# Performance work log

Hardware: AMD Instinct MI355X
Metric: run time of the kernel (lower is better)

## Reference

```python
import jax, jax.numpy as jnp
import numpy as np

B, S, H = 4, 4096, 2880
E, K = 32, 4


def setup_inputs() -> dict:
    key = jax.random.key(0)
    k1, k2 = jax.random.split(key)
    hidden_states = jax.random.normal(k1, (B, S, H), dtype=jnp.float32)
    # router weight, scaled like a typical init (std ~ 1/sqrt(H))
    weight = jax.random.normal(k2, (E, H), dtype=jnp.float32) / np.sqrt(H)
    bias = jnp.zeros((E,), dtype=jnp.float32)
    return {"hidden_states": hidden_states, "weight": weight, "bias": bias}


def reference(hidden_states, weight, bias):
    b, s, h = hidden_states.shape
    x = hidden_states.reshape(-1, h)                     # [T, H]
    logits = jnp.einsum('th,eh->te', x, weight) + bias   # [T, E]
    # select top-k logits (sorted descending), then softmax over the subset
    topk_logits, topk_idx = jax.lax.top_k(logits, K)     # [T, K]
    topk_weight = jax.nn.softmax(topk_logits.astype(jnp.float32), axis=-1)
    return topk_idx, topk_weight
```

## Files before the change

### kernel.cpp

```cpp
#include <hip/hip_runtime.h>
#include <math.h>

#define H_DIM 2880
#define E_NUM 32
#define TOPK 4
#define TT 32
#define KW 96
#define NSTG 30
#define NBUF 3
#define GRP 776
#define XB 0
#define XBS 3104
#define WB 9312
#define WBS 3104
#define SMSZ 18624
#define REDR 36
#define LGTO 4608

#define GLD16(gp, lp)                                                  \
    __builtin_amdgcn_global_load_lds(                                  \
        (const __attribute__((address_space(1))) void*)(gp),           \
        (__attribute__((address_space(3))) void*)(lp), 16, 0, 0)

__global__ __launch_bounds__(256, 2) void gate_fused(
    const float* __restrict__ x, const float* __restrict__ w,
    const float* __restrict__ bias, float* __restrict__ out, int T) {
    __shared__ float sm[SMSZ];
    const int tid = threadIdx.x;
    const int lane = tid & 63;
    const int wq = __builtin_amdgcn_readfirstlane(tid >> 6);
    const int tt = lane & 3;
    const int et = (lane >> 2) & 3;
    const int ksl = lane >> 4;
    const int t0 = blockIdx.x * TT;

    const float* gx[3]; const float* gw[3]; int lx[3], lw[3];
#pragma unroll
    for (int i = 0; i < 3; ++i) {
        const int d = i * 256 + lane * 4;
        const int r = d / KW, kk = d % KW;
        gx[i] = x + (size_t)(t0 + wq * 8 + r) * H_DIM + kk;
        gw[i] = w + (size_t)(wq * 8 + r) * H_DIM + kk;
        lx[i] = XB + wq * GRP + d;
        lw[i] = WB + wq * GRP + d;
    }

    float acc[64];
#pragma unroll
    for (int i = 0; i < 64; ++i) acc[i] = 0.f;

#pragma unroll
    for (int i = 0; i < 3; ++i) GLD16(gx[i], &sm[lx[i]]);
#pragma unroll
    for (int i = 0; i < 3; ++i) GLD16(gw[i], &sm[lw[i]]);
#pragma unroll
    for (int i = 0; i < 3; ++i) GLD16(gx[i] + KW, &sm[lx[i] + XBS]);
#pragma unroll
    for (int i = 0; i < 3; ++i) GLD16(gw[i] + KW, &sm[lw[i] + WBS]);

    const int ks = wq * 4 + ksl;
    const int koA = ks * 4;
    const int koB = 64 + ks * 2;

    int p = 0, pf = 2;
    for (int s = 0; s < NSTG; ++s) {
        if (s + 1 < NSTG) {
            asm volatile("s_waitcnt vmcnt(6)" ::: "memory");
        } else {
            asm volatile("s_waitcnt vmcnt(0)" ::: "memory");
        }
        __builtin_amdgcn_s_barrier();
        asm volatile("" ::: "memory");

        if (s + 2 < NSTG) {
            const size_t go = (size_t)(s + 2) * KW;
            const int xo = pf * XBS, wo = pf * WBS;
#pragma unroll
            for (int i = 0; i < 3; ++i) GLD16(gx[i] + go, &sm[lx[i] + xo]);
#pragma unroll
            for (int i = 0; i < 3; ++i) GLD16(gw[i] + go, &sm[lw[i] + wo]);
        }

        const float* xbp = &sm[XB + p * XBS + tt * GRP];
        const float* wbp = &sm[WB + p * WBS + et * GRP];

        float4 xa[8], wa[8];
#pragma unroll
        for (int i = 0; i < 8; ++i) xa[i] = *(const float4*)(xbp + i * KW + koA);
#pragma unroll
        for (int j = 0; j < 8; ++j) wa[j] = *(const float4*)(wbp + j * KW + koA);
#pragma unroll
        for (int i = 0; i < 8; ++i)
#pragma unroll
            for (int j = 0; j < 8; ++j)
                acc[i * 8 + j] += xa[i].x * wa[j].x + xa[i].y * wa[j].y +
                                  xa[i].z * wa[j].z + xa[i].w * wa[j].w;

        float2 x2[8], w2[8];
#pragma unroll
        for (int i = 0; i < 8; ++i) x2[i] = *(const float2*)(xbp + i * KW + koB);
#pragma unroll
        for (int j = 0; j < 8; ++j) w2[j] = *(const float2*)(wbp + j * KW + koB);
#pragma unroll
        for (int i = 0; i < 8; ++i)
#pragma unroll
            for (int j = 0; j < 8; ++j)
                acc[i * 8 + j] += x2[i].x * w2[j].x + x2[i].y * w2[j].y;

        p = (p == NBUF - 1) ? 0 : p + 1;
        pf = (pf == NBUF - 1) ? 0 : pf + 1;
    }

    __syncthreads();

#pragma unroll
    for (int d = 0; d < 64; ++d) {
        acc[d] += __shfl_xor(acc[d], 16, 64);
        acc[d] += __shfl_xor(acc[d], 32, 64);
    }

    if (ksl == 0) {
#pragma unroll
        for (int i = 0; i < 8; ++i) {
            float* rp = &sm[wq * (TT * REDR) + (tt * 8 + i) * REDR + et * 8];
            *(float4*)(rp + 0) = make_float4(acc[i * 8 + 0], acc[i * 8 + 1],
                                             acc[i * 8 + 2], acc[i * 8 + 3]);
            *(float4*)(rp + 4) = make_float4(acc[i * 8 + 4], acc[i * 8 + 5],
                                             acc[i * 8 + 6], acc[i * 8 + 7]);
        }
    }
    __syncthreads();

    {
        const int tok = tid >> 3, e4 = (tid & 7) * 4;
        float4 sg = *(const float4*)(bias + e4);
#pragma unroll
        for (int q = 0; q < 4; ++q) {
            float4 v = *(const float4*)&sm[q * (TT * REDR) + tok * REDR + e4];
            sg.x += v.x; sg.y += v.y; sg.z += v.z; sg.w += v.w;
        }
        *(float4*)&sm[LGTO + tok * REDR + e4] = sg;
    }
    __syncthreads();

    if (tid < TT) {
        const int t = t0 + tid;
        float logit[E_NUM];
#pragma unroll
        for (int j = 0; j < 8; ++j) {
            float4 v = *(const float4*)&sm[LGTO + tid * REDR + j * 4];
            logit[j * 4] = v.x; logit[j * 4 + 1] = v.y;
            logit[j * 4 + 2] = v.z; logit[j * 4 + 3] = v.w;
        }

        int idx[TOPK];
        float val[TOPK];
#pragma unroll
        for (int k = 0; k < TOPK; ++k) {
            float best = -INFINITY;
            int bi = 0;
#pragma unroll
            for (int e = 0; e < E_NUM; ++e) {
                bool taken = false;
                for (int p2 = 0; p2 < k; ++p2) taken = taken || (idx[p2] == e);
                float v = logit[e];
                if (!taken && v > best) { best = v; bi = e; }
            }
            idx[k] = bi;
            val[k] = best;
        }
        float ex[TOPK], ssum = 0.f;
#pragma unroll
        for (int k = 0; k < TOPK; ++k) { ex[k] = expf(val[k] - val[0]); ssum += ex[k]; }
        const float inv = 1.f / ssum;

        *(float4*)(out + (size_t)t * 4) =
            make_float4((float)idx[0], (float)idx[1], (float)idx[2], (float)idx[3]);
        *(float4*)(out + (size_t)T * 4 + (size_t)t * 4) =
            make_float4(ex[0] * inv, ex[1] * inv, ex[2] * inv, ex[3] * inv);
    }
}

extern "C" void kernel_launch(void* const* d_in, const int* in_sizes, int n_in,
                              void* d_out, int out_size, void* d_ws, size_t ws_size,
                              hipStream_t stream) {
    const float* x    = (const float*)d_in[0];
    const float* w    = (const float*)d_in[1];
    const float* bias = (const float*)d_in[2];
    float* out = (float*)d_out;

    const int T = in_sizes[0] / H_DIM;

    gate_fused<<<dim3(T / TT), 256, 0, stream>>>(x, w, bias, out, T);
}
```

Before: 274.9 us.

## Halve token tile to 16 and double-buffer to raise occupancy

Shrinks the per-block token tile from 32 to 16, which halves accumulators per thread (64 to 32) and roughly halves LDS use. Pipelining drops from a triple buffer with prefetch depth 2 to a double buffer that waits on all loads each stage. Launch bounds go from 2 to 4 blocks per CU, and only two waves load x. The aim is more resident waves to hide memory latency, at the cost of re-reading the router weight twice as often and a shallower prefetch.

```diff
diff --git a/kernel.cpp b/kernel.cpp
--- a/kernel.cpp
+++ b/kernel.cpp
@@ -4,25 +4,23 @@
 #define H_DIM 2880
 #define E_NUM 32
 #define TOPK 4
-#define TT 32
+#define TT 16
 #define KW 96
 #define NSTG 30
-#define NBUF 3
 #define GRP 776
-#define XB 0
-#define XBS 3104
-#define WB 9312
+#define XBS 1552
+#define WB0 3104
 #define WBS 3104
-#define SMSZ 18624
+#define SMSZ 9312
 #define REDR 36
-#define LGTO 4608
+#define LGTO 2304
 
 #define GLD16(gp, lp)                                                  \
     __builtin_amdgcn_global_load_lds(                                  \
         (const __attribute__((address_space(1))) void*)(gp),           \
         (__attribute__((address_space(3))) void*)(lp), 16, 0, 0)
 
-__global__ __launch_bounds__(256, 2) void gate_fused(
+__global__ __launch_bounds__(256, 4) void gate_fused(
     const float* __restrict__ x, const float* __restrict__ w,
     const float* __restrict__ bias, float* __restrict__ out, int T) {
     __shared__ float sm[SMSZ];
@@ -34,95 +32,85 @@
     const int ksl = lane >> 4;
     const int t0 = blockIdx.x * TT;
 
-    const float* gx[3]; const float* gw[3]; int lx[3], lw[3];
+    const float* gw[3]; int lw[3];
+    const float* gx[3]; int lx[3];
 #pragma unroll
     for (int i = 0; i < 3; ++i) {
         const int d = i * 256 + lane * 4;
         const int r = d / KW, kk = d % KW;
-        gx[i] = x + (size_t)(t0 + wq * 8 + r) * H_DIM + kk;
         gw[i] = w + (size_t)(wq * 8 + r) * H_DIM + kk;
-        lx[i] = XB + wq * GRP + d;
-        lw[i] = WB + wq * GRP + d;
+        lw[i] = WB0 + wq * GRP + d;
+        const int xr = (wq & 1) * 8 + r;
+        gx[i] = x + (size_t)(t0 + xr) * H_DIM + kk;
+        lx[i] = (wq & 1) * GRP + d;
     }
 
-    float acc[64];
+    float acc[32];
 #pragma unroll
-    for (int i = 0; i < 64; ++i) acc[i] = 0.f;
+    for (int i = 0; i < 32; ++i) acc[i] = 0.f;
 
 #pragma unroll
-    for (int i = 0; i < 3; ++i) GLD16(gx[i], &sm[lx[i]]);
+    for (int i = 0; i < 3; ++i) GLD16(gw[i], &sm[lw[i]]);
+    if (wq < 2) {
 #pragma unroll
-    for (int i = 0; i < 3; ++i) GLD16(gw[i], &sm[lw[i]]);
-#pragma unroll
-    for (int i = 0; i < 3; ++i) GLD16(gx[i] + KW, &sm[lx[i] + XBS]);
-#pragma unroll
-    for (int i = 0; i < 3; ++i) GLD16(gw[i] + KW, &sm[lw[i] + WBS]);
+        for (int i = 0; i < 3; ++i) GLD16(gx[i], &sm[lx[i]]);
+    }
 
     const int ks = wq * 4 + ksl;
     const int koA = ks * 4;
     const int koB = 64 + ks * 2;
+    const int xln = (tt >> 1) * GRP + (tt & 1) * (4 * KW);
+    const int wln = et * GRP;
 
-    int p = 0, pf = 2;
     for (int s = 0; s < NSTG; ++s) {
-        if (s + 1 < NSTG) {
-            asm volatile("s_waitcnt vmcnt(6)" ::: "memory");
-        } else {
-            asm volatile("s_waitcnt vmcnt(0)" ::: "memory");
-        }
+        asm volatile("s_waitcnt vmcnt(0)" ::: "memory");
         __builtin_amdgcn_s_barrier();
         asm volatile("" ::: "memory");
 
-        if (s + 2 < NSTG) {
-            const size_t go = (size_t)(s + 2) * KW;
-            const int xo = pf * XBS, wo = pf * WBS;
+        if (s + 1 < NSTG) {
+            const size_t go = (size_t)(s + 1) * KW;
+            const int b = (s + 1) & 1;
 #pragma unroll
-            for (int i = 0; i < 3; ++i) GLD16(gx[i] + go, &sm[lx[i] + xo]);
+            for (int i = 0; i < 3; ++i) GLD16(gw[i] + go, &sm[lw[i] + b * WBS]);
+            if (wq < 2) {
 #pragma unroll
-            for (int i = 0; i < 3; ++i) GLD16(gw[i] + go, &sm[lw[i] + wo]);
+                for (int i = 0; i < 3; ++i) GLD16(gx[i] + go, &sm[lx[i] + b * XBS]);
+            }
         }
 
-        const float* xbp = &sm[XB + p * XBS + tt * GRP];
-        const float* wbp = &sm[WB + p * WBS + et * GRP];
+        const int p = s & 1;
+        const float* xb = &sm[p * XBS + xln];
+        const float* wb = &sm[WB0 + p * WBS + wln];
 
-        float4 xa[8], wa[8];
+        float4 xa[4]; float2 xc[4];
 #pragma unroll
-        for (int i = 0; i < 8; ++i) xa[i] = *(const float4*)(xbp + i * KW + koA);
+        for (int i = 0; i < 4; ++i) xa[i] = *(const float4*)(xb + i * KW + koA);
 #pragma unroll
-        for (int j = 0; j < 8; ++j) wa[j] = *(const float4*)(wbp + j * KW + koA);
+        for (int i = 0; i < 4; ++i) xc[i] = *(const float2*)(xb + i * KW + koB);
 #pragma unroll
-        for (int i = 0; i < 8; ++i)
+        for (int j = 0; j < 8; ++j) {
+            const float4 wv = *(const float4*)(wb + j * KW + koA);
+            const float2 wc = *(const float2*)(wb + j * KW + koB);
 #pragma unroll
-            for (int j = 0; j < 8; ++j)
-                acc[i * 8 + j] += xa[i].x * wa[j].x + xa[i].y * wa[j].y +
-                                  xa[i].z * wa[j].z + xa[i].w * wa[j].w;
-
-        float2 x2[8], w2[8];
-#pragma unroll
-        for (int i = 0; i < 8; ++i) x2[i] = *(const float2*)(xbp + i * KW + koB);
-#pragma unroll
-        for (int j = 0; j < 8; ++j) w2[j] = *(const float2*)(wbp + j * KW + koB);
-#pragma unroll
-        for (int i = 0; i < 8; ++i)
-#pragma unroll
-            for (int j = 0; j < 8; ++j)
-                acc[i * 8 + j] += x2[i].x * w2[j].x + x2[i].y * w2[j].y;
-
-        p = (p == NBUF - 1) ? 0 : p + 1;
-        pf = (pf == NBUF - 1) ? 0 : pf + 1;
+            for (int i = 0; i < 4; ++i)
+                acc[i * 8 + j] += xa[i].x * wv.x + xa[i].y * wv.y +
+                                  xa[i].z * wv.z + xa[i].w * wv.w +
+                                  xc[i].x * wc.x + xc[i].y * wc.y;
+        }
     }
 
     __syncthreads();
 
 #pragma unroll
-    for (int d = 0; d < 64; ++d) {
+    for (int d = 0; d < 32; ++d) {
         acc[d] += __shfl_xor(acc[d], 16, 64);
         acc[d] += __shfl_xor(acc[d], 32, 64);
     }
 
     if (ksl == 0) {
 #pragma unroll
-        for (int i = 0; i < 8; ++i) {
-            float* rp = &sm[wq * (TT * REDR) + (tt * 8 + i) * REDR + et * 8];
+        for (int i = 0; i < 4; ++i) {
+            float* rp = &sm[wq * (TT * REDR) + (tt * 4 + i) * REDR + et * 8];
             *(float4*)(rp + 0) = make_float4(acc[i * 8 + 0], acc[i * 8 + 1],
                                              acc[i * 8 + 2], acc[i * 8 + 3]);
             *(float4*)(rp + 4) = make_float4(acc[i * 8 + 4], acc[i * 8 + 5],
@@ -131,7 +119,7 @@
     }
     __syncthreads();
 
-    {
+    if (tid < 128) {
         const int tok = tid >> 3, e4 = (tid & 7) * 4;
         float4 sg = *(const float4*)(bias + e4);
 #pragma unroll
```

New measurement: 275.5 us. About the same (+0.2%).
